# Optimization experiments

Measured on AMD Instinct MI355X. Metric: run time of the kernel, lower is better.

The kernel has to match this reference:

```python
import jax, jax.numpy as jnp
import numpy as np

B, W, L = 512, 64, 3
NODE_DIM = 172
EDGE_DIM = 172
TIME_DIM = NODE_DIM
HID = 64
EVENT_DIM = EDGE_DIM + TIME_DIM + 3  # 347
MLP_DIM = HID + 12                   # 76, if_cat=True
N_NODES = 10000
N_EDGES = 200000


def _lin_init(key, out_d, in_d):
    kw, kb = jax.random.split(key)
    s = 1.0 / np.sqrt(in_d)
    w = jax.random.uniform(kw, (out_d, in_d), minval=-s, maxval=s, dtype=jnp.float32)
    b = jax.random.uniform(kb, (out_d,), minval=-s, maxval=s, dtype=jnp.float32)
    return w, b


def setup_inputs() -> dict:
    key = jax.random.key(0)
    ks = jax.random.split(key, 24)
    inp = {}
    inp["node_idx"] = jax.random.randint(ks[0], (B, W, 2 * L), 0, N_NODES)
    inp["edge_idx"] = jax.random.randint(ks[1], (B, W, L), 0, N_EDGES)
    inp["cat_feat"] = jax.random.randint(ks[2], (B, W, 1), 0, 12)
    inp["t_records"] = jax.random.uniform(ks[3], (B, W, L), dtype=jnp.float32)
    inp["edge_identify"] = jax.random.uniform(ks[4], (B, W, L, 3), dtype=jnp.float32)
    inp["cut_time_l"] = jax.random.uniform(ks[5], (B,), dtype=jnp.float32)
    # learned tables / params
    inp["node_embed"] = jax.random.normal(ks[6], (N_NODES, NODE_DIM), dtype=jnp.float32)
    inp["edge_embed"] = jax.random.normal(ks[7], (N_EDGES, EDGE_DIM), dtype=jnp.float32)
    inp["basis_freq"] = (1.0 / 10 ** np.linspace(0, 9, TIME_DIM)).astype(np.float32)
    inp["phase"] = jnp.zeros((TIME_DIM,), dtype=jnp.float32)
    inp["lin_event_w"], inp["lin_event_b"] = _lin_init(ks[8], NODE_DIM, EVENT_DIM)
    inp["gcn_w1"], inp["gcn_b1"] = _lin_init(ks[9], HID, NODE_DIM)
    inp["gcn_w2"], inp["gcn_b2"] = _lin_init(ks[10], HID, HID)
    D2 = 2 * HID
    inp["att_w1_w"], inp["att_w1_b"] = _lin_init(ks[11], D2, D2)
    inp["att_w2_w"], _ = _lin_init(ks[12], D2, D2)
    inp["att_w2_b"] = jnp.full((D2,), 0.1, dtype=jnp.float32)
    inp["att_m1_w"], inp["att_m1_b"] = _lin_init(ks[13], HID, D2)
    inp["att_m2_w"], inp["att_m2_b"] = _lin_init(ks[14], HID, HID)
    inp["mlp_w1"], inp["mlp_b1"] = _lin_init(ks[15], MLP_DIM, MLP_DIM)
    inp["mlp_w2"], inp["mlp_b2"] = _lin_init(ks[16], HID, MLP_DIM)
    inp["mlp_w3"], inp["mlp_b3"] = _lin_init(ks[17], 1, HID)
    return inp


def _linear(x, w, b):
    return x @ w.T + b


def reference(node_idx, edge_idx, cat_feat, t_records, edge_identify, cut_time_l,
              node_embed, edge_embed, basis_freq, phase,
              lin_event_w, lin_event_b, gcn_w1, gcn_b1, gcn_w2, gcn_b2,
              att_w1_w, att_w1_b, att_w2_w, att_w2_b,
              att_m1_w, att_m1_b, att_m2_w, att_m2_b,
              mlp_w1, mlp_b1, mlp_w2, mlp_b2, mlp_w3, mlp_b3):
    # --- retrieve features (pure gathers: memory-bound) ---
    edge_f = edge_embed[edge_idx]                      # [B,W,L,E]
    delta_t = t_records[..., -1:] - t_records          # [B,W,L]
    time_f = jnp.cos(delta_t[..., None] * basis_freq + phase)  # [B,W,L,T]
    event_f = jnp.concatenate([edge_f, edge_identify, time_f], axis=-1)  # [B,W,L,EVENT_DIM]
    src_f = node_embed[node_idx[:, :, 0::2]]           # [B,W,L,NODE_DIM]
    tgt_f = node_embed[node_idx[:, :, 1::2]]

    # --- EventGCN (GINEConv-like), applied twice with src/tgt swapped ---
    event = _linear(event_f, lin_event_w, lin_event_b)  # [B,W,L,NODE_DIM]

    def gine(s, t):
        msg = jax.nn.relu(t + event)
        h = jax.nn.relu(_linear(s + msg, gcn_w1, gcn_b1))
        return _linear(h, gcn_w2, gcn_b2)               # [B,W,L,HID]

    feat = jnp.concatenate([gine(src_f, tgt_f), gine(tgt_f, src_f)], axis=-1)  # [B,W,L,2H]

    # --- walk attention (query = step 2, keys = steps 0,1) ---
    src = feat[:, :, 2:3, :]                           # [B,W,1,2H]
    tgt = feat[:, :, 0:2, :]                           # [B,W,2,2H]
    Wp = _linear(src, att_w1_w, att_w1_b)
    Wq = _linear(tgt, att_w2_w, att_w2_b)
    scores = jnp.einsum('bwqd,bwkd->bwqk', Wp, Wq)     # [B,W,1,2]
    alpha = jax.nn.softmax(scores, axis=-1)
    out = src + jnp.einsum('bwqk,bwkd->bwqd', alpha, Wq)
    h = _linear(jax.nn.relu(_linear(out, att_m1_w, att_m1_b)), att_m2_w, att_m2_b)
    src_feature = h[:, :, 0, :]                        # [B,W,HID]

    # --- category one-hot (event level) + final MLP + sigmoid ---
    cat_oh = jax.nn.one_hot(cat_feat[..., 0], 12, dtype=src_feature.dtype)  # [B,W,12]
    x = jnp.concatenate([src_feature, cat_oh], axis=-1)                      # [B,W,MLP_DIM]
    h1 = jax.nn.relu(_linear(x, mlp_w1, mlp_b1))       # dropout is identity at eval
    h2 = jax.nn.relu(_linear(h1, mlp_w2, mlp_b2))
    z = _linear(h2, mlp_w3, mlp_b3)                    # [B,W,1]
    return jax.nn.sigmoid(z)
```

## Files before the change

### kernel.cpp

```cpp
#include <hip/hip_runtime.h>
#include <hip/hip_bf16.h>
#include <math.h>

#define NW    32768
#define G     8
#define NBLK  (NW / G)
#define NT    512

#define ND    172
#define EVD   347
#define HID   64
#define D2    128
#define MLPD  76

#define W1OFF  0
#define G1OFF  (121 * 512)
#define G2OFF  (145 * 512)
#define ATTOFF (153 * 512)
#define NFRAG  217
#define WSF_BYTE_OFF 222208
#define M1OFF4 0
#define M2OFF4 2048
#define W1OFF4 3072
#define W2OFF4 4672
#define NF4    5952

#define B_EF    0
#define B_U     0
#define B_EV    9600
#define B_H     19200
#define B_FEATB 0
#define B_SRCF  6528
#define B_PQ    10624
#define B_SC    0
#define LDS_BYTES 26112

#define EFS 360
#define EVS 200
#define US  200
#define HS  72
#define FBS 136
#define SCS 204

typedef __attribute__((ext_vector_type(8))) short bf16x8;
typedef __attribute__((ext_vector_type(4))) float f32x4;

static __device__ __forceinline__ float dot4(float acc, const float4 a, const float4 b) {
  acc = fmaf(a.x, b.x, acc);
  acc = fmaf(a.y, b.y, acc);
  acc = fmaf(a.z, b.z, acc);
  acc = fmaf(a.w, b.w, acc);
  return acc;
}

static __device__ __forceinline__ short f2bf(float f) {
  union { __hip_bfloat16 h; short s; } u;
  u.h = __float2bfloat16(f);
  return u.s;
}
static __device__ __forceinline__ float bf2f(short s) {
  union { float f; unsigned u; } u;
  u.u = ((unsigned)(unsigned short)s) << 16;
  return u.f;
}

__global__ __launch_bounds__(256) void prep_weights(
    const float* __restrict__ w1, const float* __restrict__ g1,
    const float* __restrict__ g2, const float* __restrict__ a1,
    const float* __restrict__ a2, short* __restrict__ ws)
{
  const int t = blockIdx.x * 256 + threadIdx.x;
  if (t >= NFRAG * 64) return;
  const int fid  = t >> 6;
  const int lane = t & 63;
  const int q = lane >> 4, mr = lane & 15;
  bf16x8 o;
  if (fid < 121) {
    const int nt = fid / 11, ks = fid - 11 * nt;
    const int n = nt * 16 + mr, k0 = ks * 32 + q * 8;
#pragma unroll
    for (int j = 0; j < 8; ++j) {
      const int k = k0 + j;
      o[j] = (n < ND && k < EVD) ? f2bf(w1[n * EVD + k]) : (short)0;
    }
  } else if (fid < 145) {
    const int f = fid - 121, nt = f / 6, ks = f - 6 * nt;
    const int n = nt * 16 + mr, k0 = ks * 32 + q * 8;
#pragma unroll
    for (int j = 0; j < 8; ++j) {
      const int k = k0 + j;
      o[j] = (k < ND) ? f2bf(g1[n * ND + k]) : (short)0;
    }
  } else if (fid < 153) {
    const int f = fid - 145, nt = f / 2, ks = f - 2 * nt;
    const int n = nt * 16 + mr, k0 = ks * 32 + q * 8;
#pragma unroll
    for (int j = 0; j < 8; ++j) o[j] = f2bf(g2[n * HID + k0 + j]);
  } else {
    const int f = fid - 153, nt = f / 4, ks = f - 4 * nt;
    const int n = nt * 16 + mr, k0 = ks * 32 + q * 8;
    const float* src = (n < D2) ? (a1 + n * D2) : (a2 + (n - D2) * D2);
#pragma unroll
    for (int j = 0; j < 8; ++j) o[j] = f2bf(src[k0 + j]);
  }
  *(bf16x8*)&ws[(long)t * 8] = o;
}

__global__ __launch_bounds__(256) void prep_wf(
    const float* __restrict__ m1, const float* __restrict__ m2,
    const float* __restrict__ w1, const float* __restrict__ w2,
    float4* __restrict__ wf)
{
  const int t = blockIdx.x * 256 + threadIdx.x;
  if (t >= NF4) return;
  float4 o; o.x = 0.f; o.y = 0.f; o.z = 0.f; o.w = 0.f;
  if (t < M2OFF4) {
    const int kb = t >> 6, n = t & 63;
    const float* s = m1 + n * D2 + kb * 4;
    o.x = s[0]; o.y = s[1]; o.z = s[2]; o.w = s[3];
  } else if (t < W1OFF4) {
    const int u = t - M2OFF4, kb = u >> 6, n = u & 63;
    const float* s = m2 + n * HID + kb * 4;
    o.x = s[0]; o.y = s[1]; o.z = s[2]; o.w = s[3];
  } else if (t < W2OFF4) {
    const int u = t - W1OFF4, kb = u / 80, n = u - kb * 80;
    if (n < MLPD) {
#pragma unroll
      for (int j = 0; j < 4; ++j) {
        const int k = kb * 4 + j;
        ((float*)&o)[j] = (k < MLPD) ? w1[n * MLPD + k] : 0.f;
      }
    }
  } else {
    const int u = t - W2OFF4, kb = u >> 6, n = u & 63;
#pragma unroll
    for (int j = 0; j < 4; ++j) {
      const int k = kb * 4 + j;
      ((float*)&o)[j] = (k < MLPD) ? w2[n * MLPD + k] : 0.f;
    }
  }
  wf[t] = o;
}

__global__ __launch_bounds__(512, 6) void tempme_fused(
    const int*   __restrict__ node_idx,
    const int*   __restrict__ edge_idx,
    const int*   __restrict__ cat_feat,
    const float* __restrict__ t_records,
    const float* __restrict__ edge_identify,
    const float* __restrict__ node_embed,
    const float* __restrict__ edge_embed,
    const float* __restrict__ basis_freq,
    const float* __restrict__ phase,
    const float* __restrict__ lin_event_b,
    const float* __restrict__ gcn_b1,
    const float* __restrict__ gcn_b2,
    const float* __restrict__ att_w1_b,
    const float* __restrict__ att_w2_b,
    const float* __restrict__ att_m1_b,
    const float* __restrict__ att_m2_b,
    const float* __restrict__ mlp_b1,
    const float* __restrict__ mlp_b2,
    const float* __restrict__ mlp_w3,
    const float* __restrict__ mlp_b3,
    const short* __restrict__ ws,
    const float4* __restrict__ wsf,
    float*       __restrict__ out)
{
  __shared__ __align__(16) unsigned char smem[LDS_BYTES];
  short* EF    = (short*)&smem[B_EF];
  short* EV    = (short*)&smem[B_EV];
  short* U     = (short*)&smem[B_U];
  short* Hs    = (short*)&smem[B_H];
  short* FEATB = (short*)&smem[B_FEATB];
  float* SRCF  = (float*)&smem[B_SRCF];
  float* PQ    = (float*)&smem[B_PQ];
  float* SC    = (float*)&smem[B_SC];

  const int tid  = threadIdx.x;
  const int lane = tid & 63;
  const int wv   = tid >> 6;
  const int q    = lane >> 4;
  const int mr   = lane & 15;
  const int bw0  = blockIdx.x * G;

  int   eidx_[3], si_[3], ti_[3], rid_[3];
  float dt_[3];
#pragma unroll
  for (int i = 0; i < 3; ++i) {
    const int r = wv + 8 * i;
    const int g = r / 3;
    const int l = r - 3 * g;
    const int bw = bw0 + g;
    const int rid = bw * 3 + l;
    rid_[i]  = rid;
    eidx_[i] = edge_idx[rid];
    si_[i]   = node_idx[bw * 6 + 2 * l];
    ti_[i]   = node_idx[bw * 6 + 2 * l + 1];
    dt_[i]   = t_records[bw * 3 + 2] - t_records[rid];
  }

#pragma unroll
  for (int i = 0; i < 3; ++i) {
    const int r = wv + 8 * i;
    const float dt = dt_[i];
    const float* erow = edge_embed + (long)eidx_[i] * ND;
#pragma unroll
    for (int c = 0; c < 6; ++c) {
      const int k = c * 64 + lane;
      float v = 0.f;
      if (k < ND)            v = erow[k];
      else if (k < ND + 3)   v = edge_identify[rid_[i] * 3 + (k - ND)];
      else if (k < EVD) {
        const int d = k - (ND + 3);
        v = __cosf(fmaf(dt, basis_freq[d], phase[d]));
      }
      if (k < 352) EF[r * EFS + k] = f2bf(v);
    }
  }

  float ps[3][3], pt[3][3];
#pragma unroll
  for (int i = 0; i < 3; ++i) {
    const float* srow = node_embed + (long)si_[i] * ND;
    const float* trow = node_embed + (long)ti_[i] * ND;
#pragma unroll
    for (int c = 0; c < 3; ++c) {
      const int k = c * 64 + lane;
      float sv = 0.f, tv = 0.f;
      if (k < ND) { sv = srow[k]; tv = trow[k]; }
      ps[i][c] = sv;
      pt[i][c] = tv;
    }
  }
  __syncthreads();

  {
    const int a1r = (mr < 8) ? (16 + mr) : 23;
    const bool two = (wv < 3);
    f32x4 accA0 = (f32x4){0.f, 0.f, 0.f, 0.f};
    f32x4 accA1 = (f32x4){0.f, 0.f, 0.f, 0.f};
    f32x4 accB0 = (f32x4){0.f, 0.f, 0.f, 0.f};
    f32x4 accB1 = (f32x4){0.f, 0.f, 0.f, 0.f};

#pragma unroll 2
    for (int ks = 0; ks < 11; ++ks) {
      const int k0 = ks * 32 + q * 8;
      const bf16x8 a0 = *(const bf16x8*)&EF[mr * EFS + k0];
      const bf16x8 a1 = *(const bf16x8*)&EF[a1r * EFS + k0];
      {
        const bf16x8 b = *(const bf16x8*)&ws[W1OFF + ((wv * 11 + ks) * 64 + lane) * 8];
        accA0 = __builtin_amdgcn_mfma_f32_16x16x32_bf16(a0, b, accA0, 0, 0, 0);
        accA1 = __builtin_amdgcn_mfma_f32_16x16x32_bf16(a1, b, accA1, 0, 0, 0);
      }
      if (two) {
        const bf16x8 b = *(const bf16x8*)&ws[W1OFF + (((wv + 8) * 11 + ks) * 64 + lane) * 8];
        accB0 = __builtin_amdgcn_mfma_f32_16x16x32_bf16(a0, b, accB0, 0, 0, 0);
        accB1 = __builtin_amdgcn_mfma_f32_16x16x32_bf16(a1, b, accB1, 0, 0, 0);
      }
    }
    __syncthreads();
    {
      const int n = wv * 16 + mr;
      const float bo = (n < ND) ? lin_event_b[n] : 0.f;
#pragma unroll
      for (int reg = 0; reg < 4; ++reg) {
        const int m0 = q * 4 + reg;
        EV[m0 * EVS + n] = f2bf(accA0[reg] + bo);
        const int m1 = 16 + q * 4 + reg;
        if (m1 < 24) EV[m1 * EVS + n] = f2bf(accA1[reg] + bo);
      }
    }
    if (two) {
      const int n = (wv + 8) * 16 + mr;
      const float bo = (n < ND) ? lin_event_b[n] : 0.f;
#pragma unroll
      for (int reg = 0; reg < 4; ++reg) {
        const int m0 = q * 4 + reg;
        EV[m0 * EVS + n] = f2bf(accB0[reg] + bo);
        const int m1 = 16 + q * 4 + reg;
        if (m1 < 24) EV[m1 * EVS + n] = f2bf(accB1[reg] + bo);
      }
    }
  }
  __syncthreads();

  {
    float ev[3][3];
#pragma unroll
    for (int i = 0; i < 3; ++i) {
      const int r = wv + 8 * i;
#pragma unroll
      for (int c = 0; c < 3; ++c) {
        const int k = c * 64 + lane;
        ev[i][c] = (k < ND) ? bf2f(EV[r * EVS + k]) : 0.f;
      }
    }
#pragma unroll
    for (int i = 0; i < 3; ++i) {
      const int r = wv + 8 * i;
#pragma unroll
      for (int c = 0; c < 3; ++c) {
        const int k = c * 64 + lane;
        float u0v = 0.f, u1v = 0.f;
        if (k < ND) {
          const float e = ev[i][c];
          const float s = ps[i][c];
          const float t = pt[i][c];
          u0v = s + fmaxf(t + e, 0.f);
          u1v = t + fmaxf(s + e, 0.f);
        }
        U[r * US + k]        = f2bf(u0v);
        U[(24 + r) * US + k] = f2bf(u1v);
      }
    }
  }
  __syncthreads();

  {
    const int np = (wv < 4) ? 2 : 1;
#pragma unroll 1
    for (int pp = 0; pp < np; ++pp) {
      const int p = wv + 8 * pp;
      const int mtile = p >> 2, ntb = p & 3;
      const int urow = mtile * 16 + mr;
      f32x4 acc = (f32x4){0.f, 0.f, 0.f, 0.f};
#pragma unroll 2
      for (int ks = 0; ks < 6; ++ks) {
        const int k0 = ks * 32 + q * 8;
        const bf16x8 a = *(const bf16x8*)&U[urow * US + k0];
        const bf16x8 b = *(const bf16x8*)&ws[G1OFF + ((ntb * 6 + ks) * 64 + lane) * 8];
        acc = __builtin_amdgcn_mfma_f32_16x16x32_bf16(a, b, acc, 0, 0, 0);
      }
      const int j = ntb * 16 + mr;
      const float b1 = gcn_b1[j];
#pragma unroll
      for (int reg = 0; reg < 4; ++reg) {
        const int m = mtile * 16 + q * 4 + reg;
        Hs[m * HS + j] = f2bf(fmaxf(acc[reg] + b1, 0.f));
      }
    }
  }
  __syncthreads();

  {
    const int np = (wv < 4) ? 2 : 1;
#pragma unroll 1
    for (int pp = 0; pp < np; ++pp) {
      const int p = wv + 8 * pp;
      const int mtile = p >> 2, ntb = p & 3;
      const int hrow = mtile * 16 + mr;
      f32x4 acc = (f32x4){0.f, 0.f, 0.f, 0.f};
#pragma unroll
      for (int ks = 0; ks < 2; ++ks) {
        const int k0 = ks * 32 + q * 8;
        const bf16x8 a = *(const bf16x8*)&Hs[hrow * HS + k0];
        const bf16x8 b = *(const bf16x8*)&ws[G2OFF + ((ntb * 2 + ks) * 64 + lane) * 8];
        acc = __builtin_amdgcn_mfma_f32_16x16x32_bf16(a, b, acc, 0, 0, 0);
      }
      const int j = ntb * 16 + mr;
      const float b2 = gcn_b2[j];
#pragma unroll
      for (int reg = 0; reg < 4; ++reg) {
        const int m = mtile * 16 + q * 4 + reg;
        const int d = (m < 24) ? 0 : 1;
        const int r = m - 24 * d;
        const float v = acc[reg] + b2;
        const int n = d * HID + j;
        FEATB[r * FBS + n] = f2bf(v);
        if (r % 3 == 2) SRCF[(r / 3) * 128 + n] = v;
      }
    }
  }
  __syncthreads();

  {
    const int fr1 = (16 + mr < 24) ? (16 + mr) : 23;
    f32x4 acc[2][2];
#pragma unroll
    for (int tt = 0; tt < 2; ++tt)
#pragma unroll
      for (int mt = 0; mt < 2; ++mt) acc[tt][mt] = (f32x4){0.f, 0.f, 0.f, 0.f};
#pragma unroll 2
    for (int ks = 0; ks < 4; ++ks) {
      const int k0 = ks * 32 + q * 8;
      const bf16x8 a0 = *(const bf16x8*)&FEATB[mr * FBS + k0];
      const bf16x8 a1 = *(const bf16x8*)&FEATB[fr1 * FBS + k0];
#pragma unroll
      for (int tt = 0; tt < 2; ++tt) {
        const int nt = wv * 2 + tt;
        const bf16x8 b = *(const bf16x8*)&ws[ATTOFF + ((nt * 4 + ks) * 64 + lane) * 8];
        acc[tt][0] = __builtin_amdgcn_mfma_f32_16x16x32_bf16(a0, b, acc[tt][0], 0, 0, 0);
        acc[tt][1] = __builtin_amdgcn_mfma_f32_16x16x32_bf16(a1, b, acc[tt][1], 0, 0, 0);
      }
    }
#pragma unroll
    for (int tt = 0; tt < 2; ++tt) {
      const int n = (wv * 2 + tt) * 16 + mr;
      const float bias = (n < D2) ? att_w1_b[n] : att_w2_b[n - D2];
#pragma unroll
      for (int mt = 0; mt < 2; ++mt)
#pragma unroll
        for (int reg = 0; reg < 4; ++reg) {
          const int m = mt * 16 + q * 4 + reg;
          if (m < 24) {
            const int l = m % 3;
            if (l == 2) { if (n < D2)  PQ[m * 128 + n]        = acc[tt][mt][reg] + bias; }
            else        { if (n >= D2) PQ[m * 128 + (n - D2)] = acc[tt][mt][reg] + bias; }
          }
        }
    }
  }
  __syncthreads();

  {
    const int g = wv;
    float* Aw = SC + g * SCS;
    float* Bw = Aw + 128;

    {
      const float p0  = PQ[(3 * g + 2) * 128 + lane];
      const float p1  = PQ[(3 * g + 2) * 128 + 64 + lane];
      const float q00 = PQ[(3 * g + 0) * 128 + lane];
      const float q01 = PQ[(3 * g + 0) * 128 + 64 + lane];
      const float q10 = PQ[(3 * g + 1) * 128 + lane];
      const float q11 = PQ[(3 * g + 1) * 128 + 64 + lane];
      float s0 = p0 * q00 + p1 * q01;
      float s1 = p0 * q10 + p1 * q11;
#pragma unroll
      for (int off = 32; off >= 1; off >>= 1) {
        s0 += __shfl_xor(s0, off, 64);
        s1 += __shfl_xor(s1, off, 64);
      }
      const float mx = fmaxf(s0, s1);
      const float e0 = __expf(s0 - mx), e1 = __expf(s1 - mx);
      const float inv = 1.f / (e0 + e1);
      const float a0 = e0 * inv, a1 = e1 * inv;
      Aw[lane]      = SRCF[g * 128 + lane]      + a0 * q00 + a1 * q10;
      Aw[64 + lane] = SRCF[g * 128 + 64 + lane] + a0 * q01 + a1 * q11;
    }

    const float4* M1P = wsf + M1OFF4;
    const float4* M2P = wsf + M2OFF4;
    const float4* W1P = wsf + W1OFF4;
    const float4* W2P = wsf + W2OFF4;

    {
      float aa0 = 0.f, aa1 = 0.f;
#pragma unroll 4
      for (int kb = 0; kb < 32; kb += 2) {
        const float4 w0 = M1P[kb * 64 + lane];
        const float4 w1 = M1P[(kb + 1) * 64 + lane];
        const float4 x0 = *(const float4*)&Aw[kb * 4];
        const float4 x1 = *(const float4*)&Aw[kb * 4 + 4];
        aa0 = dot4(aa0, w0, x0); aa1 = dot4(aa1, w1, x1);
      }
      Bw[lane] = fmaxf(att_m1_b[lane] + aa0 + aa1, 0.f);
    }

    float hv;
    {
      float aa0 = 0.f, aa1 = 0.f;
#pragma unroll 4
      for (int kb = 0; kb < 16; kb += 2) {
        const float4 w0 = M2P[kb * 64 + lane];
        const float4 w1 = M2P[(kb + 1) * 64 + lane];
        const float4 x0 = *(const float4*)&Bw[kb * 4];
        const float4 x1 = *(const float4*)&Bw[kb * 4 + 4];
        aa0 = dot4(aa0, w0, x0); aa1 = dot4(aa1, w1, x1);
      }
      hv = att_m2_b[lane] + aa0 + aa1;
    }

    Aw[lane] = hv;
    if (lane < 16) {
      const int ca = cat_feat[bw0 + g];
      Aw[64 + lane] = (lane < 12 && ca == lane) ? 1.f : 0.f;
    }

    {
      float an = 0.f, an2 = 0.f;
      const int l2 = 64 + (lane & 15);
#pragma unroll 4
      for (int kb = 0; kb < 20; ++kb) {
        const float4 wn  = W1P[kb * 80 + lane];
        const float4 wn2 = W1P[kb * 80 + l2];
        const float4 x  = *(const float4*)&Aw[kb * 4];
        an  = dot4(an,  wn,  x);
        an2 = dot4(an2, wn2, x);
      }
      Bw[lane] = fmaxf(mlp_b1[lane] + an, 0.f);
      if (lane < 12) Bw[64 + lane] = fmaxf(mlp_b1[64 + lane] + an2, 0.f);
    }

    {
      float ha = 0.f;
#pragma unroll 4
      for (int kb = 0; kb < 20; ++kb) {
        const float4 w = W2P[kb * 64 + lane];
        const float4 x = *(const float4*)&Bw[kb * 4];
        ha = dot4(ha, w, x);
      }
      const float h2 = fmaxf(mlp_b2[lane] + ha, 0.f);
      float zz = mlp_w3[lane] * h2;
#pragma unroll
      for (int off = 32; off >= 1; off >>= 1) zz += __shfl_xor(zz, off, 64);
      if (lane == 0) out[bw0 + g] = 1.f / (1.f + __expf(-(zz + mlp_b3[0])));
    }
  }
}

extern "C" void kernel_launch(void* const* d_in, const int* in_sizes, int n_in,
                              void* d_out, int out_size, void* d_ws, size_t ws_size,
                              hipStream_t stream) {
  short* ws = (short*)d_ws;
  float4* wsf = (float4*)((char*)d_ws + WSF_BYTE_OFF);
  prep_weights<<<(NFRAG * 64 + 255) / 256, 256, 0, stream>>>(
      (const float*)d_in[10],
      (const float*)d_in[12],
      (const float*)d_in[14],
      (const float*)d_in[16],
      (const float*)d_in[18],
      ws);
  prep_wf<<<(NF4 + 255) / 256, 256, 0, stream>>>(
      (const float*)d_in[20],
      (const float*)d_in[22],
      (const float*)d_in[24],
      (const float*)d_in[26],
      wsf);
  tempme_fused<<<NBLK, NT, 0, stream>>>(
      (const int*)d_in[0],
      (const int*)d_in[1],
      (const int*)d_in[2],
      (const float*)d_in[3],
      (const float*)d_in[4],
      (const float*)d_in[6],
      (const float*)d_in[7],
      (const float*)d_in[8],
      (const float*)d_in[9],
      (const float*)d_in[11],
      (const float*)d_in[13],
      (const float*)d_in[15],
      (const float*)d_in[17],
      (const float*)d_in[19],
      (const float*)d_in[21],
      (const float*)d_in[23],
      (const float*)d_in[25],
      (const float*)d_in[27],
      (const float*)d_in[28],
      (const float*)d_in[29],
      ws, wsf,
      (float*)d_out);
}
```

Baseline: 459.2 us.

## Halve walks per block to four with 256-thread blocks and retiled MFMA work

Reduces the walks processed per block from 8 to 4 and the block size from 512 to 256 threads, halving LDS use and doubling the block count. All MFMA stages are remapped: each wave now handles a single 12-row M tile (padded to 16) with more N tiles per wave, and the row indices are clamped. The aim is better occupancy and less barrier cost per block, but MFMA rows are wasted on padding (12 of 16 used instead of 24 of 32) and the weight fragments are reread per block twice as often.

```diff
diff --git a/kernel.cpp b/kernel.cpp
--- a/kernel.cpp
+++ b/kernel.cpp
@@ -3,9 +3,9 @@
 #include <math.h>
 
 #define NW    32768
-#define G     8
+#define G     4
 #define NBLK  (NW / G)
-#define NT    512
+#define NT    256
 
 #define ND    172
 #define EVD   347
@@ -27,13 +27,13 @@
 
 #define B_EF    0
 #define B_U     0
-#define B_EV    9600
-#define B_H     19200
+#define B_EV    4800
+#define B_H     9600
 #define B_FEATB 0
-#define B_SRCF  6528
-#define B_PQ    10624
+#define B_SRCF  3264
+#define B_PQ    5312
 #define B_SC    0
-#define LDS_BYTES 26112
+#define LDS_BYTES 13056
 
 #define EFS 360
 #define EVS 200
@@ -142,7 +142,7 @@
   wf[t] = o;
 }
 
-__global__ __launch_bounds__(512, 6) void tempme_fused(
+__global__ __launch_bounds__(256) void tempme_fused(
     const int*   __restrict__ node_idx,
     const int*   __restrict__ edge_idx,
     const int*   __restrict__ cat_feat,
@@ -188,7 +188,7 @@
   float dt_[3];
 #pragma unroll
   for (int i = 0; i < 3; ++i) {
-    const int r = wv + 8 * i;
+    const int r = wv + 4 * i;
     const int g = r / 3;
     const int l = r - 3 * g;
     const int bw = bw0 + g;
@@ -202,7 +202,7 @@
 
 #pragma unroll
   for (int i = 0; i < 3; ++i) {
-    const int r = wv + 8 * i;
+    const int r = wv + 4 * i;
     const float dt = dt_[i];
     const float* erow = edge_embed + (long)eidx_[i] * ND;
 #pragma unroll
@@ -236,27 +236,27 @@
   __syncthreads();
 
   {
-    const int a1r = (mr < 8) ? (16 + mr) : 23;
-    const bool two = (wv < 3);
-    f32x4 accA0 = (f32x4){0.f, 0.f, 0.f, 0.f};
-    f32x4 accA1 = (f32x4){0.f, 0.f, 0.f, 0.f};
-    f32x4 accB0 = (f32x4){0.f, 0.f, 0.f, 0.f};
-    f32x4 accB1 = (f32x4){0.f, 0.f, 0.f, 0.f};
+    const int ar = (mr < 12) ? mr : 11;
+    const bool three = (wv < 3);
+    f32x4 accA = (f32x4){0.f, 0.f, 0.f, 0.f};
+    f32x4 accB = (f32x4){0.f, 0.f, 0.f, 0.f};
+    f32x4 accC = (f32x4){0.f, 0.f, 0.f, 0.f};
 
 #pragma unroll 2
     for (int ks = 0; ks < 11; ++ks) {
       const int k0 = ks * 32 + q * 8;
-      const bf16x8 a0 = *(const bf16x8*)&EF[mr * EFS + k0];
-      const bf16x8 a1 = *(const bf16x8*)&EF[a1r * EFS + k0];
+      const bf16x8 a0 = *(const bf16x8*)&EF[ar * EFS + k0];
       {
         const bf16x8 b = *(const bf16x8*)&ws[W1OFF + ((wv * 11 + ks) * 64 + lane) * 8];
-        accA0 = __builtin_amdgcn_mfma_f32_16x16x32_bf16(a0, b, accA0, 0, 0, 0);
-        accA1 = __builtin_amdgcn_mfma_f32_16x16x32_bf16(a1, b, accA1, 0, 0, 0);
-      }
-      if (two) {
+        accA = __builtin_amdgcn_mfma_f32_16x16x32_bf16(a0, b, accA, 0, 0, 0);
+      }
+      {
+        const bf16x8 b = *(const bf16x8*)&ws[W1OFF + (((wv + 4) * 11 + ks) * 64 + lane) * 8];
+        accB = __builtin_amdgcn_mfma_f32_16x16x32_bf16(a0, b, accB, 0, 0, 0);
+      }
+      if (three) {
         const bf16x8 b = *(const bf16x8*)&ws[W1OFF + (((wv + 8) * 11 + ks) * 64 + lane) * 8];
-        accB0 = __builtin_amdgcn_mfma_f32_16x16x32_bf16(a0, b, accB0, 0, 0, 0);
-        accB1 = __builtin_amdgcn_mfma_f32_16x16x32_bf16(a1, b, accB1, 0, 0, 0);
+        accC = __builtin_amdgcn_mfma_f32_16x16x32_bf16(a0, b, accC, 0, 0, 0);
       }
     }
     __syncthreads();
@@ -265,21 +265,26 @@
       const float bo = (n < ND) ? lin_event_b[n] : 0.f;
 #pragma unroll
       for (int reg = 0; reg < 4; ++reg) {
-        const int m0 = q * 4 + reg;
-        EV[m0 * EVS + n] = f2bf(accA0[reg] + bo);
-        const int m1 = 16 + q * 4 + reg;
-        if (m1 < 24) EV[m1 * EVS + n] = f2bf(accA1[reg] + bo);
-      }
-    }
-    if (two) {
+        const int m = q * 4 + reg;
+        if (m < 12) EV[m * EVS + n] = f2bf(accA[reg] + bo);
+      }
+    }
+    {
+      const int n = (wv + 4) * 16 + mr;
+      const float bo = (n < ND) ? lin_event_b[n] : 0.f;
+#pragma unroll
+      for (int reg = 0; reg < 4; ++reg) {
+        const int m = q * 4 + reg;
+        if (m < 12) EV[m * EVS + n] = f2bf(accB[reg] + bo);
+      }
+    }
+    if (three) {
       const int n = (wv + 8) * 16 + mr;
       const float bo = (n < ND) ? lin_event_b[n] : 0.f;
 #pragma unroll
       for (int reg = 0; reg < 4; ++reg) {
-        const int m0 = q * 4 + reg;
-        EV[m0 * EVS + n] = f2bf(accB0[reg] + bo);
-        const int m1 = 16 + q * 4 + reg;
-        if (m1 < 24) EV[m1 * EVS + n] = f2bf(accB1[reg] + bo);
+        const int m = q * 4 + reg;
+        if (m < 12) EV[m * EVS + n] = f2bf(accC[reg] + bo);
       }
     }
   }
@@ -289,7 +294,7 @@
     float ev[3][3];
 #pragma unroll
     for (int i = 0; i < 3; ++i) {
-      const int r = wv + 8 * i;
+      const int r = wv + 4 * i;
 #pragma unroll
       for (int c = 0; c < 3; ++c) {
         const int k = c * 64 + lane;
@@ -298,7 +303,7 @@
     }
 #pragma unroll
     for (int i = 0; i < 3; ++i) {
-      const int r = wv + 8 * i;
+      const int r = wv + 4 * i;
 #pragma unroll
       for (int c = 0; c < 3; ++c) {
         const int k = c * 64 + lane;
@@ -311,19 +316,19 @@
           u1v = t + fmaxf(s + e, 0.f);
         }
         U[r * US + k]        = f2bf(u0v);
-        U[(24 + r) * US + k] = f2bf(u1v);
+        U[(12 + r) * US + k] = f2bf(u1v);
       }
     }
   }
   __syncthreads();
 
   {
-    const int np = (wv < 4) ? 2 : 1;
 #pragma unroll 1
-    for (int pp = 0; pp < np; ++pp) {
-      const int p = wv + 8 * pp;
+    for (int pp = 0; pp < 2; ++pp) {
+      const int p = wv + 4 * pp;
       const int mtile = p >> 2, ntb = p & 3;
-      const int urow = mtile * 16 + mr;
+      const int urow0 = mtile * 16 + mr;
+      const int urow  = (urow0 > 23) ? 23 : urow0;
       f32x4 acc = (f32x4){0.f, 0.f, 0.f, 0.f};
 #pragma unroll 2
       for (int ks = 0; ks < 6; ++ks) {
@@ -337,19 +342,19 @@
 #pragma unroll
       for (int reg = 0; reg < 4; ++reg) {
         const int m = mtile * 16 + q * 4 + reg;
-        Hs[m * HS + j] = f2bf(fmaxf(acc[reg] + b1, 0.f));
+        if (m < 24) Hs[m * HS + j] = f2bf(fmaxf(acc[reg] + b1, 0.f));
       }
     }
   }
   __syncthreads();
 
   {
-    const int np = (wv < 4) ? 2 : 1;
 #pragma unroll 1
-    for (int pp = 0; pp < np; ++pp) {
-      const int p = wv + 8 * pp;
+    for (int pp = 0; pp < 2; ++pp) {
+      const int p = wv + 4 * pp;
       const int mtile = p >> 2, ntb = p & 3;
-      const int hrow = mtile * 16 + mr;
+      const int hrow0 = mtile * 16 + mr;
+      const int hrow  = (hrow0 > 23) ? 23 : hrow0;
       f32x4 acc = (f32x4){0.f, 0.f, 0.f, 0.f};
 #pragma unroll
       for (int ks = 0; ks < 2; ++ks) {
@@ -363,52 +368,48 @@
 #pragma unroll
       for (int reg = 0; reg < 4; ++reg) {
         const int m = mtile * 16 + q * 4 + reg;
-        const int d = (m < 24) ? 0 : 1;
-        const int r = m - 24 * d;
-        const float v = acc[reg] + b2;
-        const int n = d * HID + j;
-        FEATB[r * FBS + n] = f2bf(v);
-        if (r % 3 == 2) SRCF[(r / 3) * 128 + n] = v;
+        if (m < 24) {
+          const int d = (m < 12) ? 0 : 1;
+          const int r = m - 12 * d;
+          const float v = acc[reg] + b2;
+          const int n = d * HID + j;
+          FEATB[r * FBS + n] = f2bf(v);
+          if (r % 3 == 2) SRCF[(r / 3) * 128 + n] = v;
+        }
       }
     }
   }
   __syncthreads();
 
   {
-    const int fr1 = (16 + mr < 24) ? (16 + mr) : 23;
-    f32x4 acc[2][2];
-#pragma unroll
-    for (int tt = 0; tt < 2; ++tt)
-#pragma unroll
-      for (int mt = 0; mt < 2; ++mt) acc[tt][mt] = (f32x4){0.f, 0.f, 0.f, 0.f};
+    const int ar = (mr < 12) ? mr : 11;
+    f32x4 acc[4];
+#pragma unroll
+    for (int tt = 0; tt < 4; ++tt) acc[tt] = (f32x4){0.f, 0.f, 0.f, 0.f};
 #pragma unroll 2
     for (int ks = 0; ks < 4; ++ks) {
       const int k0 = ks * 32 + q * 8;
-      const bf16x8 a0 = *(const bf16x8*)&FEATB[mr * FBS + k0];
-      const bf16x8 a1 = *(const bf16x8*)&FEATB[fr1 * FBS + k0];
-#pragma unroll
-      for (int tt = 0; tt < 2; ++tt) {
-        const int nt = wv * 2 + tt;
+      const bf16x8 a0 = *(const bf16x8*)&FEATB[ar * FBS + k0];
+#pragma unroll
+      for (int tt = 0; tt < 4; ++tt) {
+        const int nt = wv * 4 + tt;
         const bf16x8 b = *(const bf16x8*)&ws[ATTOFF + ((nt * 4 + ks) * 64 + lane) * 8];
-        acc[tt][0] = __builtin_amdgcn_mfma_f32_16x16x32_bf16(a0, b, acc[tt][0], 0, 0, 0);
-        acc[tt][1] = __builtin_amdgcn_mfma_f32_16x16x32_bf16(a1, b, acc[tt][1], 0, 0, 0);
-      }
-    }
-#pragma unroll
-    for (int tt = 0; tt < 2; ++tt) {
-      const int n = (wv * 2 + tt) * 16 + mr;
+        acc[tt] = __builtin_amdgcn_mfma_f32_16x16x32_bf16(a0, b, acc[tt], 0, 0, 0);
+      }
+    }
+#pragma unroll
+    for (int tt = 0; tt < 4; ++tt) {
+      const int n = (wv * 4 + tt) * 16 + mr;
       const float bias = (n < D2) ? att_w1_b[n] : att_w2_b[n - D2];
 #pragma unroll
-      for (int mt = 0; mt < 2; ++mt)
-#pragma unroll
-        for (int reg = 0; reg < 4; ++reg) {
-          const int m = mt * 16 + q * 4 + reg;
-          if (m < 24) {
-            const int l = m % 3;
-            if (l == 2) { if (n < D2)  PQ[m * 128 + n]        = acc[tt][mt][reg] + bias; }
-            else        { if (n >= D2) PQ[m * 128 + (n - D2)] = acc[tt][mt][reg] + bias; }
-          }
+      for (int reg = 0; reg < 4; ++reg) {
+        const int m = q * 4 + reg;
+        if (m < 12) {
+          const int l = m % 3;
+          if (l == 2) { if (n < D2)  PQ[m * 128 + n]        = acc[tt][reg] + bias; }
+          else        { if (n >= D2) PQ[m * 128 + (n - D2)] = acc[tt][reg] + bias; }
         }
+      }
     }
   }
   __syncthreads();
```

New measurement: 486.9 us. 6.0% more time.
